# Kernel optimization log

Measured on AMD Instinct MI355X. Metric: run time of the kernel, lower is better.

## Reference

```python
import jax, jax.numpy as jnp
import numpy as np

B, S, NH, NKV, D = 2, 2048, 32, 8, 128

def setup_inputs() -> dict:
    key = jax.random.key(0)
    kq, kk, kv = jax.random.split(key, 3)
    query = jax.random.normal(kq, (B, S, NH, D), dtype=jnp.float32)
    k_ = jax.random.normal(kk, (B, S, NKV, D), dtype=jnp.float32)
    v_ = jax.random.normal(kv, (B, S, NKV, D), dtype=jnp.float32)
    # causal additive mask, broadcastable to [B, NH, S, S]
    causal = jnp.tril(jnp.ones((S, S), dtype=bool))
    attn_mask = jnp.where(causal, 0.0, -1e9).astype(jnp.float32)[None, None]
    return {"query": query, "key": k_, "value": v_, "attn_mask": attn_mask}

def reference(query, key, value, attn_mask):
    nh, nkv = query.shape[-2], key.shape[-2]
    # [B, S, H, D] -> [B, H, S, D]
    q = jnp.swapaxes(query, -3, -2)
    k = jnp.swapaxes(key, -3, -2)
    v = jnpp_swap(value) if False else jnp.swapaxes(value, -3, -2)
    qpk = nh // nkv
    if qpk > 1:
        k = jnp.repeat(k, qpk, axis=-3)
        v = jnp.repeat(v, qpk, axis=-3)
    scale = q.shape[-1] ** (-0.5)
    # [B, H, Sq, Sk]
    score = jnp.einsum('bhqd,bhkd->bhqk', q, k) * scale
    score = score + attn_mask
    probs = jax.nn.softmax(score.astype(jnp.float32), axis=-1).astype(q.dtype)
    out = jnp.einsum('bhqk,bhkd->bhqd', probs, v)
    # [B, H, S, D] -> [B, S, H, D]
    return jnp.swapaxes(out, 1, 2)
```

## Files before the change

### kernel.cpp

```cpp
#include <hip/hip_runtime.h>
#include <hip/hip_bf16.h>

#define B_    2
#define S_    2048
#define NH_   32
#define NKV_  8
#define D_    128
#define QBLK  128
#define KVBLK 64

#define KVH_STRIDE 524288u
#define V_WS_OFF   8388608u

typedef __bf16 bf16x8 __attribute__((ext_vector_type(8)));
typedef float  f32x16 __attribute__((ext_vector_type(16)));
typedef unsigned short u16x4 __attribute__((ext_vector_type(4)));
typedef unsigned int   u32x4 __attribute__((ext_vector_type(4)));

typedef const __attribute__((address_space(1))) void* gptr_t;
typedef __attribute__((address_space(3))) void*       lptr_t;

__device__ inline unsigned short f2bfu(float f) {
    unsigned u = __builtin_bit_cast(unsigned, f);
    u += 0x7fffu + ((u >> 16) & 1u);
    return (unsigned short)(u >> 16);
}
__device__ inline __bf16 f2bf(float f) {
    unsigned short s = f2bfu(f);
    return __builtin_bit_cast(__bf16, s);
}
__device__ inline unsigned packbf(float lo, float hi) {
    return (unsigned)f2bfu(lo) | ((unsigned)f2bfu(hi) << 16);
}

__device__ inline void* kaddr(unsigned short* base, int row, int byteInRow) {
    return (void*)((char*)base + row * 256 + (byteInRow ^ ((row & 7) << 4)));
}
__device__ inline void* vaddr(unsigned short* base, int row, int byteInRow) {
    return (void*)((char*)base + row * 128 + (byteInRow ^ ((row & 7) << 4)));
}

__global__ __launch_bounds__(256)
void convert_k(const float* __restrict__ kin, unsigned short* __restrict__ kout) {
    const int g = blockIdx.x * 256 + threadIdx.x;
    const size_t o = (size_t)g * 4;
    const int d   = (int)(o & 127);
    const int k   = (int)((o >> 7) & 2047);
    const int kvh = (int)((o >> 18) & 7);
    const int b   = (int)(o >> 21);
    const float* src = kin + (((size_t)(b * 2048 + k)) * 8 + kvh) * 128 + d;
    float4 x = *reinterpret_cast<const float4*>(src);
    u16x4 u = { f2bfu(x.x), f2bfu(x.y), f2bfu(x.z), f2bfu(x.w) };
    *reinterpret_cast<u16x4*>(kout + o) = u;
}

__global__ __launch_bounds__(256)
void convert_v(const float* __restrict__ vin, unsigned short* __restrict__ vout) {
    __shared__ unsigned short vl[64][136];
    const int t  = threadIdx.x;
    const int bb = blockIdx.x;
    const int j  = bb & 31;
    const int bk = bb >> 5;
    const int b  = bk >> 3, kvh = bk & 7;
    const float* base = vin + (((size_t)(b * 2048 + j * 64)) * 8 + kvh) * 128;
    #pragma unroll
    for (int i = 0; i < 8; ++i) {
        const int row = i * 8 + (t >> 5), c4 = t & 31;
        float4 x = *reinterpret_cast<const float4*>(base + (size_t)row * 1024 + c4 * 4);
        u16x4 u = { f2bfu(x.x), f2bfu(x.y), f2bfu(x.z), f2bfu(x.w) };
        *reinterpret_cast<u16x4*>(&vl[row][c4 * 4]) = u;
    }
    __syncthreads();
    unsigned short* out = vout + (size_t)bb * 8192;
    #pragma unroll
    for (int it = 0; it < 4; ++it) {
        const int c = it * 256 + t;
        const int d = c >> 3, k0 = (c & 7) * 8;
        u16x4 lo = { vl[k0 + 0][d], vl[k0 + 1][d], vl[k0 + 2][d], vl[k0 + 3][d] };
        u16x4 hi = { vl[k0 + 4][d], vl[k0 + 5][d], vl[k0 + 6][d], vl[k0 + 7][d] };
        *reinterpret_cast<u16x4*>(out + (size_t)d * 64 + k0)     = lo;
        *reinterpret_cast<u16x4*>(out + (size_t)d * 64 + k0 + 4) = hi;
    }
}

__global__ __launch_bounds__(256, 2)
void sdpa_fwd(const float* __restrict__ qg, const unsigned short* __restrict__ kws,
              const unsigned short* __restrict__ vws, float* __restrict__ og)
{
    __shared__ __align__(16) unsigned short Kb[2][8192];
    __shared__ __align__(16) unsigned short Vb[2][8192];

    const int bx  = blockIdx.x;
    const int swz = (bx & 7) * 64 + (bx >> 3);
    const int p   = swz & 7;
    const int h   = (swz >> 3) & 31;
    const int b   = swz >> 8;
    const int kvh = h >> 2;
    const int bk  = b * 8 + kvh;

    const int t   = threadIdx.x;
    const int w   = t >> 6;
    const int l   = t & 63;
    const int l32 = l & 31;
    const int lh  = l >> 5;

    const float scale = 0.08838834764831845f;

    const int koff = ((t >> 4) << 8) + ((((t & 15) << 4)) ^ (((t >> 4) & 7) << 4));
    const int voff = ((t >> 3) << 7) + ((((t & 7) << 4)) ^ (((t >> 3) & 7) << 4));
    const char* Khead = (const char*)kws + (size_t)bk * KVH_STRIDE;
    const char* Vhead = (const char*)vws + (size_t)bk * KVH_STRIDE;

    #pragma unroll 1
    for (int pass = 0; pass < 2; ++pass) {
        const int qt     = pass ? p : (15 - p);
        const int qmin_w = qt * QBLK + w * 32;
        const int qgl    = qmin_w + l32;

        bf16x8 qf[8];
        {
            const float* Qp = qg + (((size_t)b * S_ + qgl) * NH_ + h) * D_;
            #pragma unroll
            for (int dc = 0; dc < 8; ++dc) {
                const int d0 = dc * 16 + lh * 8;
                float4 a = *reinterpret_cast<const float4*>(Qp + d0);
                float4 c = *reinterpret_cast<const float4*>(Qp + d0 + 4);
                bf16x8 f;
                f[0] = f2bf(a.x * scale); f[1] = f2bf(a.y * scale);
                f[2] = f2bf(a.z * scale); f[3] = f2bf(a.w * scale);
                f[4] = f2bf(c.x * scale); f[5] = f2bf(c.y * scale);
                f[6] = f2bf(c.z * scale); f[7] = f2bf(c.w * scale);
                qf[dc] = f;
            }
        }

        f32x16 acc[4] = {};
        float mrow = -INFINITY, lrow = 0.0f;

        auto issue = [&](int j, int c) {
            const char* ks = Khead + (size_t)j * 16384 + koff;
            const char* vs = Vhead + (size_t)j * 16384 + voff;
            char* kl = (char*)&Kb[c][0] + t * 16;
            char* vl = (char*)&Vb[c][0] + t * 16;
            #pragma unroll
            for (int i = 0; i < 4; ++i) {
                __builtin_amdgcn_global_load_lds((gptr_t)(ks + i * 4096),
                                                 (lptr_t)(kl + i * 4096), 16, 0, 0);
                __builtin_amdgcn_global_load_lds((gptr_t)(vs + i * 4096),
                                                 (lptr_t)(vl + i * 4096), 16, 0, 0);
            }
        };

        __syncthreads();
        issue(0, 0);
        const int jmax = 2 * qt + 1;

        for (int j = 0; j <= jmax; ++j) {
            const int cur = j & 1;
            const int jbase = j * KVBLK;

            __builtin_amdgcn_s_barrier();
            __builtin_amdgcn_sched_barrier(0);
            if (j < jmax) {
                issue(j + 1, cur ^ 1);
                asm volatile("s_waitcnt vmcnt(8)" ::: "memory");
            } else {
                asm volatile("s_waitcnt vmcnt(0)" ::: "memory");
            }
            __builtin_amdgcn_s_barrier();
            __builtin_amdgcn_sched_barrier(0);

            if (jbase <= qmin_w + 31) {
                unsigned short* kbuf = &Kb[cur][0];
                unsigned short* vbuf = &Vb[cur][0];

                f32x16 sc0 = {}, sc1 = {};
                __builtin_amdgcn_s_setprio(1);
                #pragma unroll
                for (int dc = 0; dc < 8; ++dc) {
                    bf16x8 kf0 = *reinterpret_cast<const bf16x8*>(
                        kaddr(kbuf, l32, dc * 32 + lh * 16));
                    sc0 = __builtin_amdgcn_mfma_f32_32x32x16_bf16(kf0, qf[dc], sc0, 0, 0, 0);
                    bf16x8 kf1 = *reinterpret_cast<const bf16x8*>(
                        kaddr(kbuf, 32 + l32, dc * 32 + lh * 16));
                    sc1 = __builtin_amdgcn_mfma_f32_32x32x16_bf16(kf1, qf[dc], sc1, 0, 0, 0);
                }
                __builtin_amdgcn_s_setprio(0);

                if (jbase + (KVBLK - 1) > qmin_w) {
                    #pragma unroll
                    for (int r = 0; r < 16; ++r) {
                        const int kk = jbase + (r & 3) + 8 * (r >> 2) + 4 * lh;
                        if (kk > qgl)      sc0[r] = -INFINITY;
                        if (kk + 32 > qgl) sc1[r] = -INFINITY;
                    }
                }

                float mt = -INFINITY;
                #pragma unroll
                for (int r = 0; r < 16; ++r) mt = fmaxf(mt, fmaxf(sc0[r], sc1[r]));
                mt = fmaxf(mt, __shfl_xor(mt, 32));
                const float mnew = fmaxf(mrow, mt);
                if (!__all(mnew - mrow <= 8.0f)) {
                    const float resc = __expf(mrow - mnew);
                    lrow *= resc;
                    #pragma unroll
                    for (int dt = 0; dt < 4; ++dt) acc[dt] *= resc;
                    mrow = mnew;
                }
                float ps = 0.0f;
                #pragma unroll
                for (int r = 0; r < 16; ++r) {
                    sc0[r] = __expf(sc0[r] - mrow);
                    sc1[r] = __expf(sc1[r] - mrow);
                    ps += sc0[r] + sc1[r];
                }
                ps += __shfl_xor(ps, 32);
                lrow += ps;

                bf16x8 pa[4];
                #pragma unroll
                for (int g = 0; g < 4; ++g) {
                    float p0, p1, p2, p3, p4, p5, p6, p7;
                    if (g == 0) { p0=sc0[0]; p1=sc0[1]; p2=sc0[2]; p3=sc0[3];
                                  p4=sc0[4]; p5=sc0[5]; p6=sc0[6]; p7=sc0[7]; }
                    else if (g == 1) { p0=sc0[8];  p1=sc0[9];  p2=sc0[10]; p3=sc0[11];
                                       p4=sc0[12]; p5=sc0[13]; p6=sc0[14]; p7=sc0[15]; }
                    else if (g == 2) { p0=sc1[0]; p1=sc1[1]; p2=sc1[2]; p3=sc1[3];
                                       p4=sc1[4]; p5=sc1[5]; p6=sc1[6]; p7=sc1[7]; }
                    else { p0=sc1[8];  p1=sc1[9];  p2=sc1[10]; p3=sc1[11];
                           p4=sc1[12]; p5=sc1[13]; p6=sc1[14]; p7=sc1[15]; }
                    unsigned a0 = packbf(p0, p1), b0 = packbf(p4, p5);
                    unsigned a1 = packbf(p2, p3), b1 = packbf(p6, p7);
                    auto s02 = __builtin_amdgcn_permlane32_swap((int)a0, (int)b0, false, false);
                    auto s13 = __builtin_amdgcn_permlane32_swap((int)a1, (int)b1, false, false);
                    u32x4 dw = { (unsigned)s02[0], (unsigned)s13[0],
                                 (unsigned)s02[1], (unsigned)s13[1] };
                    pa[g] = __builtin_bit_cast(bf16x8, dw);
                }

                __builtin_amdgcn_s_setprio(1);
                #pragma unroll
                for (int kc = 0; kc < 4; ++kc) {
                    #pragma unroll
                    for (int dt = 0; dt < 4; ++dt) {
                        bf16x8 vf = *reinterpret_cast<const bf16x8*>(
                            vaddr(vbuf, dt * 32 + l32, kc * 32 + lh * 16));
                        acc[dt] = __builtin_amdgcn_mfma_f32_32x32x16_bf16(vf, pa[kc], acc[dt], 0, 0, 0);
                    }
                }
                __builtin_amdgcn_s_setprio(0);
            }
        }

        const float invl = 1.0f / lrow;
        float* Op = og + (((size_t)b * S_ + qgl) * NH_ + h) * D_;
        #pragma unroll
        for (int dt = 0; dt < 4; ++dt) {
            #pragma unroll
            for (int rg = 0; rg < 4; ++rg) {
                float4 st;
                st.x = acc[dt][rg * 4 + 0] * invl;
                st.y = acc[dt][rg * 4 + 1] * invl;
                st.z = acc[dt][rg * 4 + 2] * invl;
                st.w = acc[dt][rg * 4 + 3] * invl;
                *reinterpret_cast<float4*>(Op + dt * 32 + rg * 8 + lh * 4) = st;
            }
        }
    }
}

extern "C" void kernel_launch(void* const* d_in, const int* in_sizes, int n_in,
                              void* d_out, int out_size, void* d_ws, size_t ws_size,
                              hipStream_t stream) {
    const float* q = (const float*)d_in[0];
    const float* k = (const float*)d_in[1];
    const float* v = (const float*)d_in[2];
    float* out = (float*)d_out;
    unsigned short* kws = (unsigned short*)d_ws;
    unsigned short* vws = (unsigned short*)((char*)d_ws + V_WS_OFF);

    convert_k<<<dim3(4096), 256, 0, stream>>>(k, kws);
    convert_v<<<dim3(512),  256, 0, stream>>>(v, vws);
    sdpa_fwd <<<dim3(512),  256, 0, stream>>>(q, kws, vws, out);
}
```

Baseline: 120.9 us.

## Single-buffer V, one q-tile per block, raise occupancy to three blocks per CU

Drops the paired-q-tile loop so each block handles one query tile, doubling the grid and ordering blocks from largest causal work to smallest. V goes from a double buffer to a single buffer loaded within the same iteration, with an extra wait and barrier between QK/softmax and PV. This cuts LDS use so launch bounds can request three blocks per CU. The aim is more concurrent waves to hide latency, at the cost of exposing V load latency and losing the pairing that balanced causal work across blocks.

```diff
diff --git a/kernel.cpp b/kernel.cpp
--- a/kernel.cpp
+++ b/kernel.cpp
@@ -83,19 +83,19 @@
     }
 }
 
-__global__ __launch_bounds__(256, 2)
+__global__ __launch_bounds__(256, 3)
 void sdpa_fwd(const float* __restrict__ qg, const unsigned short* __restrict__ kws,
               const unsigned short* __restrict__ vws, float* __restrict__ og)
 {
     __shared__ __align__(16) unsigned short Kb[2][8192];
-    __shared__ __align__(16) unsigned short Vb[2][8192];
+    __shared__ __align__(16) unsigned short Vb[8192];
 
     const int bx  = blockIdx.x;
-    const int swz = (bx & 7) * 64 + (bx >> 3);
-    const int p   = swz & 7;
-    const int h   = (swz >> 3) & 31;
-    const int b   = swz >> 8;
-    const int kvh = h >> 2;
+    const int qt  = 15 - (bx >> 6);
+    const int r   = bx & 63;
+    const int kvh = r & 7;
+    const int h   = kvh * 4 + ((r >> 3) & 3);
+    const int b   = (r >> 5) & 1;
     const int bk  = b * 8 + kvh;
 
     const int t   = threadIdx.x;
@@ -105,167 +105,171 @@
     const int lh  = l >> 5;
 
     const float scale = 0.08838834764831845f;
+    const int qmin_w = qt * QBLK + w * 32;
+    const int qgl    = qmin_w + l32;
 
     const int koff = ((t >> 4) << 8) + ((((t & 15) << 4)) ^ (((t >> 4) & 7) << 4));
     const int voff = ((t >> 3) << 7) + ((((t & 7) << 4)) ^ (((t >> 3) & 7) << 4));
     const char* Khead = (const char*)kws + (size_t)bk * KVH_STRIDE;
     const char* Vhead = (const char*)vws + (size_t)bk * KVH_STRIDE;
 
-    #pragma unroll 1
-    for (int pass = 0; pass < 2; ++pass) {
-        const int qt     = pass ? p : (15 - p);
-        const int qmin_w = qt * QBLK + w * 32;
-        const int qgl    = qmin_w + l32;
-
-        bf16x8 qf[8];
-        {
-            const float* Qp = qg + (((size_t)b * S_ + qgl) * NH_ + h) * D_;
+    bf16x8 qf[8];
+    {
+        const float* Qp = qg + (((size_t)b * S_ + qgl) * NH_ + h) * D_;
+        #pragma unroll
+        for (int dc = 0; dc < 8; ++dc) {
+            const int d0 = dc * 16 + lh * 8;
+            float4 a = *reinterpret_cast<const float4*>(Qp + d0);
+            float4 c = *reinterpret_cast<const float4*>(Qp + d0 + 4);
+            bf16x8 f;
+            f[0] = f2bf(a.x * scale); f[1] = f2bf(a.y * scale);
+            f[2] = f2bf(a.z * scale); f[3] = f2bf(a.w * scale);
+            f[4] = f2bf(c.x * scale); f[5] = f2bf(c.y * scale);
+            f[6] = f2bf(c.z * scale); f[7] = f2bf(c.w * scale);
+            qf[dc] = f;
+        }
+    }
+
+    f32x16 acc[4] = {};
+    float mrow = -INFINITY, lrow = 0.0f;
+
+    auto issueK = [&](int j, int c) {
+        const char* ks = Khead + (size_t)j * 16384 + koff;
+        char* kl = (char*)&Kb[c][0] + t * 16;
+        #pragma unroll
+        for (int i = 0; i < 4; ++i)
+            __builtin_amdgcn_global_load_lds((gptr_t)(ks + i * 4096),
+                                             (lptr_t)(kl + i * 4096), 16, 0, 0);
+    };
+    auto issueV = [&](int j) {
+        const char* vs = Vhead + (size_t)j * 16384 + voff;
+        char* vl = (char*)&Vb[0] + t * 16;
+        #pragma unroll
+        for (int i = 0; i < 4; ++i)
+            __builtin_amdgcn_global_load_lds((gptr_t)(vs + i * 4096),
+                                             (lptr_t)(vl + i * 4096), 16, 0, 0);
+    };
+
+    issueK(0, 0);
+    const int jmax = 2 * qt + 1;
+
+    for (int j = 0; j <= jmax; ++j) {
+        const int cur = j & 1;
+        const int jbase = j * KVBLK;
+        const bool live = (jbase <= qmin_w + 31);
+
+        __builtin_amdgcn_s_barrier();
+        __builtin_amdgcn_sched_barrier(0);
+        issueV(j);
+        if (j < jmax) {
+            issueK(j + 1, cur ^ 1);
+            asm volatile("s_waitcnt vmcnt(8)" ::: "memory");
+        } else {
+            asm volatile("s_waitcnt vmcnt(4)" ::: "memory");
+        }
+        __builtin_amdgcn_s_barrier();
+        __builtin_amdgcn_sched_barrier(0);
+
+        f32x16 sc0 = {}, sc1 = {};
+        bf16x8 pa[4];
+        if (live) {
+            unsigned short* kbuf = &Kb[cur][0];
+            __builtin_amdgcn_s_setprio(1);
             #pragma unroll
             for (int dc = 0; dc < 8; ++dc) {
-                const int d0 = dc * 16 + lh * 8;
-                float4 a = *reinterpret_cast<const float4*>(Qp + d0);
-                float4 c = *reinterpret_cast<const float4*>(Qp + d0 + 4);
-                bf16x8 f;
-                f[0] = f2bf(a.x * scale); f[1] = f2bf(a.y * scale);
-                f[2] = f2bf(a.z * scale); f[3] = f2bf(a.w * scale);
-                f[4] = f2bf(c.x * scale); f[5] = f2bf(c.y * scale);
-                f[6] = f2bf(c.z * scale); f[7] = f2bf(c.w * scale);
-                qf[dc] = f;
-            }
-        }
-
-        f32x16 acc[4] = {};
-        float mrow = -INFINITY, lrow = 0.0f;
-
-        auto issue = [&](int j, int c) {
-            const char* ks = Khead + (size_t)j * 16384 + koff;
-            const char* vs = Vhead + (size_t)j * 16384 + voff;
-            char* kl = (char*)&Kb[c][0] + t * 16;
-            char* vl = (char*)&Vb[c][0] + t * 16;
-            #pragma unroll
-            for (int i = 0; i < 4; ++i) {
-                __builtin_amdgcn_global_load_lds((gptr_t)(ks + i * 4096),
-                                                 (lptr_t)(kl + i * 4096), 16, 0, 0);
-                __builtin_amdgcn_global_load_lds((gptr_t)(vs + i * 4096),
-                                                 (lptr_t)(vl + i * 4096), 16, 0, 0);
-            }
-        };
-
-        __syncthreads();
-        issue(0, 0);
-        const int jmax = 2 * qt + 1;
-
-        for (int j = 0; j <= jmax; ++j) {
-            const int cur = j & 1;
-            const int jbase = j * KVBLK;
-
-            __builtin_amdgcn_s_barrier();
-            __builtin_amdgcn_sched_barrier(0);
-            if (j < jmax) {
-                issue(j + 1, cur ^ 1);
-                asm volatile("s_waitcnt vmcnt(8)" ::: "memory");
-            } else {
-                asm volatile("s_waitcnt vmcnt(0)" ::: "memory");
-            }
-            __builtin_amdgcn_s_barrier();
-            __builtin_amdgcn_sched_barrier(0);
-
-            if (jbase <= qmin_w + 31) {
-                unsigned short* kbuf = &Kb[cur][0];
-                unsigned short* vbuf = &Vb[cur][0];
-
-                f32x16 sc0 = {}, sc1 = {};
-                __builtin_amdgcn_s_setprio(1);
+                bf16x8 kf0 = *reinterpret_cast<const bf16x8*>(
+                    kaddr(kbuf, l32, dc * 32 + lh * 16));
+                sc0 = __builtin_amdgcn_mfma_f32_32x32x16_bf16(kf0, qf[dc], sc0, 0, 0, 0);
+                bf16x8 kf1 = *reinterpret_cast<const bf16x8*>(
+                    kaddr(kbuf, 32 + l32, dc * 32 + lh * 16));
+                sc1 = __builtin_amdgcn_mfma_f32_32x32x16_bf16(kf1, qf[dc], sc1, 0, 0, 0);
+            }
+            __builtin_amdgcn_s_setprio(0);
+
+            if (jbase + (KVBLK - 1) > qmin_w) {
                 #pragma unroll
-                for (int dc = 0; dc < 8; ++dc) {
-                    bf16x8 kf0 = *reinterpret_cast<const bf16x8*>(
-                        kaddr(kbuf, l32, dc * 32 + lh * 16));
-                    sc0 = __builtin_amdgcn_mfma_f32_32x32x16_bf16(kf0, qf[dc], sc0, 0, 0, 0);
-                    bf16x8 kf1 = *reinterpret_cast<const bf16x8*>(
-                        kaddr(kbuf, 32 + l32, dc * 32 + lh * 16));
-                    sc1 = __builtin_amdgcn_mfma_f32_32x32x16_bf16(kf1, qf[dc], sc1, 0, 0, 0);
+                for (int rr = 0; rr < 16; ++rr) {
+                    const int kk = jbase + (rr & 3) + 8 * (rr >> 2) + 4 * lh;
+                    if (kk > qgl)      sc0[rr] = -INFINITY;
+                    if (kk + 32 > qgl) sc1[rr] = -INFINITY;
                 }
-                __builtin_amdgcn_s_setprio(0);
-
-                if (jbase + (KVBLK - 1) > qmin_w) {
-                    #pragma unroll
-                    for (int r = 0; r < 16; ++r) {
-                        const int kk = jbase + (r & 3) + 8 * (r >> 2) + 4 * lh;
-                        if (kk > qgl)      sc0[r] = -INFINITY;
-                        if (kk + 32 > qgl) sc1[r] = -INFINITY;
-                    }
+            }
+
+            float mt = -INFINITY;
+            #pragma unroll
+            for (int rr = 0; rr < 16; ++rr) mt = fmaxf(mt, fmaxf(sc0[rr], sc1[rr]));
+            mt = fmaxf(mt, __shfl_xor(mt, 32));
+            const float mnew = fmaxf(mrow, mt);
+            if (!__all(mnew - mrow <= 8.0f)) {
+                const float resc = __expf(mrow - mnew);
+                lrow *= resc;
+                #pragma unroll
+                for (int dt = 0; dt < 4; ++dt) acc[dt] *= resc;
+                mrow = mnew;
+            }
+            float ps = 0.0f;
+            #pragma unroll
+            for (int rr = 0; rr < 16; ++rr) {
+                sc0[rr] = __expf(sc0[rr] - mrow);
+                sc1[rr] = __expf(sc1[rr] - mrow);
+                ps += sc0[rr] + sc1[rr];
+            }
+            ps += __shfl_xor(ps, 32);
+            lrow += ps;
+
+            #pragma unroll
+            for (int g = 0; g < 4; ++g) {
+                float p0, p1, p2, p3, p4, p5, p6, p7;
+                if (g == 0) { p0=sc0[0]; p1=sc0[1]; p2=sc0[2]; p3=sc0[3];
+                              p4=sc0[4]; p5=sc0[5]; p6=sc0[6]; p7=sc0[7]; }
+                else if (g == 1) { p0=sc0[8];  p1=sc0[9];  p2=sc0[10]; p3=sc0[11];
+                                   p4=sc0[12]; p5=sc0[13]; p6=sc0[14]; p7=sc0[15]; }
+                else if (g == 2) { p0=sc1[0]; p1=sc1[1]; p2=sc1[2]; p3=sc1[3];
+                                   p4=sc1[4]; p5=sc1[5]; p6=sc1[6]; p7=sc1[7]; }
+                else { p0=sc1[8];  p1=sc1[9];  p2=sc1[10]; p3=sc1[11];
+                       p4=sc1[12]; p5=sc1[13]; p6=sc1[14]; p7=sc1[15]; }
+                unsigned a0 = packbf(p0, p1), b0 = packbf(p4, p5);
+                unsigned a1 = packbf(p2, p3), b1 = packbf(p6, p7);
+                auto s02 = __builtin_amdgcn_permlane32_swap((int)a0, (int)b0, false, false);
+                auto s13 = __builtin_amdgcn_permlane32_swap((int)a1, (int)b1, false, false);
+                u32x4 dw = { (unsigned)s02[0], (unsigned)s13[0],
+                             (unsigned)s02[1], (unsigned)s13[1] };
+                pa[g] = __builtin_bit_cast(bf16x8, dw);
+            }
+        }
+
+        if (j < jmax) asm volatile("s_waitcnt vmcnt(4)" ::: "memory");
+        else          asm volatile("s_waitcnt vmcnt(0)" ::: "memory");
+        __builtin_amdgcn_s_barrier();
+        __builtin_amdgcn_sched_barrier(0);
+
+        if (live) {
+            __builtin_amdgcn_s_setprio(1);
+            #pragma unroll
+            for (int kc = 0; kc < 4; ++kc) {
+                #pragma unroll
+                for (int dt = 0; dt < 4; ++dt) {
+                    bf16x8 vf = *reinterpret_cast<const bf16x8*>(
+                        vaddr(&Vb[0], dt * 32 + l32, kc * 32 + lh * 16));
+                    acc[dt] = __builtin_amdgcn_mfma_f32_32x32x16_bf16(vf, pa[kc], acc[dt], 0, 0, 0);
                 }
-
-                float mt = -INFINITY;
-                #pragma unroll
-                for (int r = 0; r < 16; ++r) mt = fmaxf(mt, fmaxf(sc0[r], sc1[r]));
-                mt = fmaxf(mt, __shfl_xor(mt, 32));
-                const float mnew = fmaxf(mrow, mt);
-                if (!__all(mnew - mrow <= 8.0f)) {
-                    const float resc = __expf(mrow - mnew);
-                    lrow *= resc;
-                    #pragma unroll
-                    for (int dt = 0; dt < 4; ++dt) acc[dt] *= resc;
-                    mrow = mnew;
-                }
-                float ps = 0.0f;
-                #pragma unroll
-                for (int r = 0; r < 16; ++r) {
-                    sc0[r] = __expf(sc0[r] - mrow);
-                    sc1[r] = __expf(sc1[r] - mrow);
-                    ps += sc0[r] + sc1[r];
-                }
-                ps += __shfl_xor(ps, 32);
-                lrow += ps;
-
-                bf16x8 pa[4];
-                #pragma unroll
-                for (int g = 0; g < 4; ++g) {
-                    float p0, p1, p2, p3, p4, p5, p6, p7;
-                    if (g == 0) { p0=sc0[0]; p1=sc0[1]; p2=sc0[2]; p3=sc0[3];
-                                  p4=sc0[4]; p5=sc0[5]; p6=sc0[6]; p7=sc0[7]; }
-                    else if (g == 1) { p0=sc0[8];  p1=sc0[9];  p2=sc0[10]; p3=sc0[11];
-                                       p4=sc0[12]; p5=sc0[13]; p6=sc0[14]; p7=sc0[15]; }
-                    else if (g == 2) { p0=sc1[0]; p1=sc1[1]; p2=sc1[2]; p3=sc1[3];
-                                       p4=sc1[4]; p5=sc1[5]; p6=sc1[6]; p7=sc1[7]; }
-                    else { p0=sc1[8];  p1=sc1[9];  p2=sc1[10]; p3=sc1[11];
-                           p4=sc1[12]; p5=sc1[13]; p6=sc1[14]; p7=sc1[15]; }
-                    unsigned a0 = packbf(p0, p1), b0 = packbf(p4, p5);
-                    unsigned a1 = packbf(p2, p3), b1 = packbf(p6, p7);
-                    auto s02 = __builtin_amdgcn_permlane32_swap((int)a0, (int)b0, false, false);
-                    auto s13 = __builtin_amdgcn_permlane32_swap((int)a1, (int)b1, false, false);
-                    u32x4 dw = { (unsigned)s02[0], (unsigned)s13[0],
-                                 (unsigned)s02[1], (unsigned)s13[1] };
-                    pa[g] = __builtin_bit_cast(bf16x8, dw);
-                }
-
-                __builtin_amdgcn_s_setprio(1);
-                #pragma unroll
-                for (int kc = 0; kc < 4; ++kc) {
-                    #pragma unroll
-                    for (int dt = 0; dt < 4; ++dt) {
-                        bf16x8 vf = *reinterpret_cast<const bf16x8*>(
-                            vaddr(vbuf, dt * 32 + l32, kc * 32 + lh * 16));
-                        acc[dt] = __builtin_amdgcn_mfma_f32_32x32x16_bf16(vf, pa[kc], acc[dt], 0, 0, 0);
-                    }
-                }
-                __builtin_amdgcn_s_setprio(0);
-            }
-        }
-
-        const float invl = 1.0f / lrow;
-        float* Op = og + (((size_t)b * S_ + qgl) * NH_ + h) * D_;
-        #pragma unroll
-        for (int dt = 0; dt < 4; ++dt) {
-            #pragma unroll
-            for (int rg = 0; rg < 4; ++rg) {
-                float4 st;
-                st.x = acc[dt][rg * 4 + 0] * invl;
-                st.y = acc[dt][rg * 4 + 1] * invl;
-                st.z = acc[dt][rg * 4 + 2] * invl;
-                st.w = acc[dt][rg * 4 + 3] * invl;
-                *reinterpret_cast<float4*>(Op + dt * 32 + rg * 8 + lh * 4) = st;
-            }
+            }
+            __builtin_amdgcn_s_setprio(0);
+        }
+    }
+
+    const float invl = 1.0f / lrow;
+    float* Op = og + (((size_t)b * S_ + qgl) * NH_ + h) * D_;
+    #pragma unroll
+    for (int dt = 0; dt < 4; ++dt) {
+        #pragma unroll
+        for (int rg = 0; rg < 4; ++rg) {
+            float4 st;
+            st.x = acc[dt][rg * 4 + 0] * invl;
+            st.y = acc[dt][rg * 4 + 1] * invl;
+            st.z = acc[dt][rg * 4 + 2] * invl;
+            st.w = acc[dt][rg * 4 + 3] * invl;
+            *reinterpret_cast<float4*>(Op + dt * 32 + rg * 8 + lh * 4) = st;
         }
     }
 }
@@ -282,5 +286,5 @@
 
     convert_k<<<dim3(4096), 256, 0, stream>>>(k, kws);
     convert_v<<<dim3(512),  256, 0, stream>>>(v, vws);
-    sdpa_fwd <<<dim3(512),  256, 0, stream>>>(q, kws, vws, out);
-}
+    sdpa_fwd <<<dim3(1024), 256, 0, stream>>>(q, kws, vws, out);
+}
```

Result: no change. 122.2 us (+1.0%).
